# Performance work log

Measured on AMD Instinct MI355X. Metric: run time of the kernel, lower is better.

Reference implementation:

```python
import jax, jax.numpy as jnp
import numpy as np

N = 100000      # num_nodes
R = 8           # num_relations
D = 128         # node feature size
EMB = 128       # embedding_size
E = 1600000     # num edges
B = 16384       # batch of triples


def setup_inputs() -> dict:
    key = jax.random.key(0)
    ks = jax.random.split(key, 10)
    edge_src = jax.random.randint(ks[0], (E,), 0, N, dtype=jnp.int32)
    edge_dst = jax.random.randint(ks[1], (E,), 0, N, dtype=jnp.int32)
    edge_rel = jax.random.randint(ks[2], (E,), 0, R, dtype=jnp.int32)
    tri_nodes = jax.random.randint(ks[3], (B, 2), 0, N, dtype=jnp.int32)
    tri_rel = jax.random.randint(ks[4], (B,), 0, R, dtype=jnp.int32)
    X = jax.random.normal(ks[5], (N, D), dtype=jnp.float32)            # frozen node features
    W_rel = jax.random.normal(ks[6], (R, D, EMB), dtype=jnp.float32) * (1.0 / np.sqrt(D))
    W_self = jax.random.normal(ks[7], (D, EMB), dtype=jnp.float32) * (1.0 / np.sqrt(D))
    b = jnp.zeros((EMB,), dtype=jnp.float32)
    rel_emb = jax.random.normal(ks[8], (R, EMB), dtype=jnp.float32) * (1.0 / np.sqrt(EMB))  # xavier-ish
    return {"X": X, "W_rel": W_rel, "W_self": W_self, "b": b, "rel_emb": rel_emb,
            "edge_src": edge_src, "edge_dst": edge_dst, "edge_rel": edge_rel,
            "tri_nodes": tri_nodes, "tri_rel": tri_rel}


def _rgcn_layer(X, W_rel, W_self, b, edge_src, edge_dst, edge_rel):
    # per-relation transformed features: [R, N, EMB]
    XW = jnp.einsum('nd,rde->rne', X, W_rel)
    # gather per-edge messages: [E, EMB]
    msg = XW[edge_rel, edge_src]
    # RGCN normalization 1/c_{i,r}: count of (dst, rel) pairs
    comb = edge_dst.astype(jnp.int32) * R + edge_rel
    cnt = jax.ops.segment_sum(jnp.ones_like(comb, dtype=jnp.float32), comb, num_segments=N * R)
    norm = 1.0 / jnp.maximum(cnt[comb], 1.0)
    agg = jax.ops.segment_sum(msg * norm[:, None], edge_dst, num_segments=N)  # [N, EMB]
    return jax.nn.relu(agg + X @ W_self + b)


def reference(X, W_rel, W_self, b, rel_emb, edge_src, edge_dst, edge_rel, tri_nodes, tri_rel):
    H = _rgcn_layer(X, W_rel, W_self, b, edge_src, edge_dst, edge_rel)  # [N, EMB]
    subj = H[tri_nodes[:, 0]]          # [B, EMB]
    obj = H[tri_nodes[:, 1]]           # [B, EMB]
    rel = rel_emb[tri_rel]             # [B, EMB]
    scores = jnp.sum(subj * rel * obj, axis=1, keepdims=True)  # [B, 1]
    return scores
```

## Files before the change

kernel.cpp:

```cpp
#include <hip/hip_runtime.h>

typedef float f32x4 __attribute__((ext_vector_type(4)));
typedef short bf16x8 __attribute__((ext_vector_type(8)));

__device__ __forceinline__ unsigned short f2bf(float f) {
  unsigned int u = __float_as_uint(f);
  u += 0x7FFFu + ((u >> 16) & 1u);
  return (unsigned short)(u >> 16);
}
__device__ __forceinline__ float bflo(unsigned int u) {
  return __uint_as_float(u << 16);
}
__device__ __forceinline__ float bfhi(unsigned int u) {
  return __uint_as_float(u & 0xFFFF0000u);
}

__global__ void k_build_map(const int* __restrict__ tri_nodes, int* __restrict__ map,
                            int* __restrict__ uniq, int* __restrict__ counter, int n) {
  int i = blockIdx.x * blockDim.x + threadIdx.x;
  if (i >= n) return;
  int node = tri_nodes[i];
  int old = atomicCAS(&map[node], -1, -2);
  if (old == -1) {
    int mid = atomicAdd(counter, 1);
    uniq[mid] = node;
    map[node] = mid;
  }
}

__global__ void k_count(const int* __restrict__ edst, const int* __restrict__ erel,
                        const int* __restrict__ map, int* __restrict__ cnt_c, int E) {
  int i = blockIdx.x * blockDim.x + threadIdx.x;
  if (i >= E) return;
  int mid = map[edst[i]];
  if (mid >= 0) atomicAdd(&cnt_c[mid * 8 + erel[i]], 1);
}

__global__ __launch_bounds__(256) void k_scan_s1(const int* __restrict__ cnt_c,
                                                 int* __restrict__ bsum) {
  __shared__ int sh[256];
  int tid = threadIdx.x;
  int base = blockIdx.x * 1024 + tid * 4;
  int s = cnt_c[base] + cnt_c[base + 1] + cnt_c[base + 2] + cnt_c[base + 3];
  sh[tid] = s;
  __syncthreads();
  for (int o = 1; o < 256; o <<= 1) {
    int x = (tid >= o) ? sh[tid - o] : 0;
    __syncthreads();
    sh[tid] += x;
    __syncthreads();
  }
  if (tid == 255) bsum[blockIdx.x] = sh[255];
}
__global__ __launch_bounds__(256) void k_scan_s2(int* __restrict__ bsum,
                                                 int* __restrict__ seg_start, int M) {
  __shared__ int sh[256];
  int tid = threadIdx.x;
  int v = bsum[tid];
  sh[tid] = v;
  __syncthreads();
  for (int o = 1; o < 256; o <<= 1) {
    int x = (tid >= o) ? sh[tid - o] : 0;
    __syncthreads();
    sh[tid] += x;
    __syncthreads();
  }
  bsum[tid] = sh[tid] - v;
  if (tid == 255) seg_start[M] = sh[255];
}
__global__ __launch_bounds__(256) void k_scan_s3(const int* __restrict__ cnt_c,
                                                 const int* __restrict__ bsum,
                                                 int* __restrict__ seg_start,
                                                 int* __restrict__ seg_ofs) {
  __shared__ int sh[256];
  int tid = threadIdx.x;
  int base = blockIdx.x * 1024 + tid * 4;
  int c0 = cnt_c[base], c1 = cnt_c[base + 1], c2 = cnt_c[base + 2], c3 = cnt_c[base + 3];
  int s = c0 + c1 + c2 + c3;
  sh[tid] = s;
  __syncthreads();
  for (int o = 1; o < 256; o <<= 1) {
    int x = (tid >= o) ? sh[tid - o] : 0;
    __syncthreads();
    sh[tid] += x;
    __syncthreads();
  }
  int run = bsum[blockIdx.x] + sh[tid] - s;
  seg_start[base] = run; seg_ofs[base] = run; run += c0;
  seg_start[base + 1] = run; seg_ofs[base + 1] = run; run += c1;
  seg_start[base + 2] = run; seg_ofs[base + 2] = run; run += c2;
  seg_start[base + 3] = run; seg_ofs[base + 3] = run;
}

__global__ void k_scatter(const int* __restrict__ esrc, const int* __restrict__ edst,
                          const int* __restrict__ erel, const int* __restrict__ map,
                          int* __restrict__ seg_ofs, int* __restrict__ s_src, int E) {
  int i = blockIdx.x * blockDim.x + threadIdx.x;
  if (i >= E) return;
  int mid = map[edst[i]];
  if (mid >= 0) {
    int comb = mid * 8 + erel[i];
    int pos = atomicAdd(&seg_ofs[comb], 1);
    s_src[pos] = esrc[i];
  }
}

__global__ void k_cvt_w(const float* __restrict__ W_rel, const float* __restrict__ W_self,
                        unsigned short* __restrict__ Wf) {
  int i = blockIdx.x * 256 + threadIdx.x;
  if (i >= 9 * 16384) return;
  int j = i & 7;
  int tmp = i >> 3;
  int col = tmp & 127;
  int ku = (tmp >> 7) & 15;
  int r = tmp >> 11;
  int d = ku * 8 + j;
  float v = (r < 8) ? W_rel[r * 16384 + d * 128 + col] : W_self[d * 128 + col];
  Wf[i] = f2bf(v);
}

__global__ void k_cvt_x(const float* __restrict__ X, unsigned short* __restrict__ X16,
                        int total8) {
  int i = blockIdx.x * 256 + threadIdx.x;
  if (i >= total8) return;
  const float4* s = (const float4*)(X + (size_t)i * 8);
  float4 v0 = s[0], v1 = s[1];
  uint4 p;
  p.x = (unsigned int)f2bf(v0.x) | ((unsigned int)f2bf(v0.y) << 16);
  p.y = (unsigned int)f2bf(v0.z) | ((unsigned int)f2bf(v0.w) << 16);
  p.z = (unsigned int)f2bf(v1.x) | ((unsigned int)f2bf(v1.y) << 16);
  p.w = (unsigned int)f2bf(v1.z) | ((unsigned int)f2bf(v1.w) << 16);
  ((uint4*)X16)[i] = p;
}

template <int XMODE>
__global__ __launch_bounds__(256) void k_fused(
    const float* __restrict__ X, const unsigned short* __restrict__ X16,
    const unsigned short* __restrict__ Wf, const float* __restrict__ bvec,
    const int* __restrict__ uniq, const int* __restrict__ counter,
    const int* __restrict__ seg_start, const int* __restrict__ s_src,
    float* __restrict__ Hacc) {
  __shared__ __align__(16) unsigned short a_lds[16 * 128];
  __shared__ int lds_src[768];

  int nm = *counter;
  int mid0 = blockIdx.x * 16;
  if (mid0 >= nm) return;

  int t = threadIdx.x;
  int er = t >> 4, seg = t & 15;
  int lane = t & 63, l15 = lane & 15, lg = lane >> 4;
  int wc = t >> 6;
  int mid = mid0 + er;

  int i0 = seg_start[mid0 * 8];
  int range = seg_start[mid0 * 8 + 128] - i0;
  for (int j = t; j < range && j < 768; j += 256) lds_src[j] = s_src[i0 + j];
  bool fits = (range <= 768);

  f32x4 acc[2];
  {
    f32x4 z = {0.f, 0.f, 0.f, 0.f};
    acc[0] = z; acc[1] = z;
  }

  for (int r = 0; r < 9; ++r) {
    __syncthreads();

    {
      float aa[8];
#pragma unroll
      for (int q = 0; q < 8; ++q) aa[q] = 0.f;

      auto addrow = [&](int sidx) {
        if (XMODE == 0) {
          const float4* xr = (const float4*)(X + (size_t)sidx * 128) + seg * 2;
          float4 v0 = xr[0], v1 = xr[1];
          aa[0] += v0.x; aa[1] += v0.y; aa[2] += v0.z; aa[3] += v0.w;
          aa[4] += v1.x; aa[5] += v1.y; aa[6] += v1.z; aa[7] += v1.w;
        } else {
          uint4 u = *(const uint4*)(X16 + (size_t)sidx * 128 + seg * 8);
          aa[0] += bflo(u.x); aa[1] += bfhi(u.x);
          aa[2] += bflo(u.y); aa[3] += bfhi(u.y);
          aa[4] += bflo(u.z); aa[5] += bfhi(u.z);
          aa[6] += bflo(u.w); aa[7] += bfhi(u.w);
        }
      };

      if (r < 8) {
        int comb = mid * 8 + r;
        int s0 = seg_start[comb], s1 = seg_start[comb + 1];
        int cnt = s1 - s0;
        if (fits) {
          int o = s0 - i0, oe = s1 - i0;
          for (; o + 2 <= oe; o += 2) {
            int ia = lds_src[o], ib = lds_src[o + 1];
            addrow(ia);
            addrow(ib);
          }
          if (o < oe) addrow(lds_src[o]);
        } else {
          int e = s0;
          for (; e + 2 <= s1; e += 2) {
            int ia = s_src[e], ib = s_src[e + 1];
            addrow(ia);
            addrow(ib);
          }
          if (e < s1) addrow(s_src[e]);
        }
        if (cnt > 1) {
          float sc = 1.0f / (float)cnt;
#pragma unroll
          for (int q = 0; q < 8; ++q) aa[q] *= sc;
        }
      } else if (mid < nm) {
        addrow(uniq[mid]);
      }
      uint4 p;
      p.x = (unsigned int)f2bf(aa[0]) | ((unsigned int)f2bf(aa[1]) << 16);
      p.y = (unsigned int)f2bf(aa[2]) | ((unsigned int)f2bf(aa[3]) << 16);
      p.z = (unsigned int)f2bf(aa[4]) | ((unsigned int)f2bf(aa[5]) << 16);
      p.w = (unsigned int)f2bf(aa[6]) | ((unsigned int)f2bf(aa[7]) << 16);
      *(uint4*)&a_lds[(((er * 16 + seg) ^ (er & 7)) * 8)] = p;
    }
    __syncthreads();

    const unsigned short* wf = Wf + r * 16384;
#pragma unroll
    for (int kb = 0; kb < 4; ++kb) {
      int ku = kb * 4 + lg;
      bf16x8 af = *(const bf16x8*)&a_lds[((l15 * 16 + ku) ^ (l15 & 7)) * 8];
#pragma unroll
      for (int n = 0; n < 2; ++n) {
        int col = wc * 32 + n * 16 + l15;
        bf16x8 bfr = *(const bf16x8*)(wf + ((size_t)(ku * 128 + col)) * 8);
        acc[n] = __builtin_amdgcn_mfma_f32_16x16x32_bf16(af, bfr, acc[n], 0, 0, 0);
      }
    }
  }

#pragma unroll
  for (int n = 0; n < 2; ++n) {
    int col = wc * 32 + n * 16 + l15;
    float bv = bvec[col];
#pragma unroll
    for (int q = 0; q < 4; ++q) {
      int row = mid0 + lg * 4 + q;
      float v = acc[n][q] + bv;
      Hacc[(size_t)row * 128 + col] = v > 0.f ? v : 0.f;
    }
  }
}

__global__ void k_score(const float* __restrict__ H, const int* __restrict__ map,
                        const float* __restrict__ rel_emb, const int* __restrict__ tri_nodes,
                        const int* __restrict__ tri_rel, float* __restrict__ out, int B) {
  int w = (blockIdx.x * blockDim.x + threadIdx.x) >> 6;
  int lane = threadIdx.x & 63;
  if (w >= B) return;
  int s = map[tri_nodes[w * 2]];
  int o = map[tri_nodes[w * 2 + 1]];
  const float* hs = H + (size_t)s * 128;
  const float* ho = H + (size_t)o * 128;
  const float* rr = rel_emb + (size_t)tri_rel[w] * 128;
  float p = hs[lane] * ho[lane] * rr[lane] + hs[lane + 64] * ho[lane + 64] * rr[lane + 64];
#pragma unroll
  for (int ofs = 32; ofs > 0; ofs >>= 1) p += __shfl_down(p, ofs);
  if (lane == 0) out[w] = p;
}

extern "C" void kernel_launch(void* const* d_in, const int* in_sizes, int n_in,
                              void* d_out, int out_size, void* d_ws, size_t ws_size,
                              hipStream_t stream) {
  const float* X       = (const float*)d_in[0];
  const float* W_rel   = (const float*)d_in[1];
  const float* W_self  = (const float*)d_in[2];
  const float* bvec    = (const float*)d_in[3];
  const float* rel_emb = (const float*)d_in[4];
  const int* edge_src  = (const int*)d_in[5];
  const int* edge_dst  = (const int*)d_in[6];
  const int* edge_rel  = (const int*)d_in[7];
  const int* tri_nodes = (const int*)d_in[8];
  const int* tri_rel   = (const int*)d_in[9];

  int N  = in_sizes[0] / 128;
  int E  = in_sizes[5];
  int nt = in_sizes[8];
  int B  = in_sizes[9];
  int M  = nt * 8;

  char* ws = (char*)d_ws;
  int* map       = (int*)ws;
  int* counter   = map + N;
  int* uniq      = counter + 64;
  int* cnt_c     = uniq + nt;
  int* seg_start = cnt_c + M;
  int* seg_ofs   = seg_start + M + 64;
  int* bsum      = seg_ofs + M;
  int* s_src     = bsum + 256;
  float* Hacc    = (float*)(s_src + E);
  unsigned short* Wf  = (unsigned short*)cnt_c;
  unsigned short* X16 = (unsigned short*)(Hacc + (size_t)nt * 128);
  size_t need_big = ((char*)(X16 + (size_t)N * 128)) - ws;
  bool bigws = ws_size >= need_big;

  hipMemsetAsync(map, 0xFF, (size_t)N * 4, stream);
  hipMemsetAsync(counter, 0, 64 * 4, stream);
  hipMemsetAsync(cnt_c, 0, (size_t)M * 4, stream);

  int eblocks = (E + 255) / 256;
  k_build_map<<<(nt + 255) / 256, 256, 0, stream>>>(tri_nodes, map, uniq, counter, nt);
  k_count<<<eblocks, 256, 0, stream>>>(edge_dst, edge_rel, map, cnt_c, E);
  k_scan_s1<<<256, 256, 0, stream>>>(cnt_c, bsum);
  k_scan_s2<<<1, 256, 0, stream>>>(bsum, seg_start, M);
  k_scan_s3<<<256, 256, 0, stream>>>(cnt_c, bsum, seg_start, seg_ofs);
  k_cvt_w<<<(9 * 16384 + 255) / 256, 256, 0, stream>>>(W_rel, W_self, Wf);
  k_scatter<<<eblocks, 256, 0, stream>>>(edge_src, edge_dst, edge_rel, map, seg_ofs,
                                         s_src, E);
  if (bigws) {
    k_cvt_x<<<(N * 16 + 255) / 256, 256, 0, stream>>>(X, X16, N * 16);
    k_fused<1><<<nt / 16, 256, 0, stream>>>(X, X16, Wf, bvec, uniq, counter,
                                            seg_start, s_src, Hacc);
  } else {
    k_fused<0><<<nt / 16, 256, 0, stream>>>(X, X16, Wf, bvec, uniq, counter,
                                            seg_start, s_src, Hacc);
  }
  k_score<<<(B * 64 + 255) / 256, 256, 0, stream>>>(Hacc, map, rel_emb, tri_nodes,
                                                    tri_rel, (float*)d_out, B);
}
```

Before: 132.9 us.

## Fuse X bf16 conversion into count pass and compact edges for scatter

```diff
diff --git a/kernel.cpp b/kernel.cpp
--- a/kernel.cpp
+++ b/kernel.cpp
@@ -28,12 +28,42 @@
   }
 }
 
-__global__ void k_count(const int* __restrict__ edst, const int* __restrict__ erel,
-                        const int* __restrict__ map, int* __restrict__ cnt_c, int E) {
-  int i = blockIdx.x * blockDim.x + threadIdx.x;
-  if (i >= E) return;
-  int mid = map[edst[i]];
-  if (mid >= 0) atomicAdd(&cnt_c[mid * 8 + erel[i]], 1);
+__global__ void k_count(const int* __restrict__ esrc, const int* __restrict__ edst,
+                        const int* __restrict__ erel, const int* __restrict__ map,
+                        int* __restrict__ cnt_c, int E,
+                        const float* __restrict__ X, unsigned short* __restrict__ X16,
+                        int total8, int2* __restrict__ c_pk, int* __restrict__ wcount) {
+  int t = threadIdx.x;
+  int i = blockIdx.x * 256 + t;
+  if (i < total8) {
+    const float4* s = (const float4*)(X + (size_t)i * 8);
+    float4 v0 = s[0], v1 = s[1];
+    uint4 p;
+    p.x = (unsigned int)f2bf(v0.x) | ((unsigned int)f2bf(v0.y) << 16);
+    p.y = (unsigned int)f2bf(v0.z) | ((unsigned int)f2bf(v0.w) << 16);
+    p.z = (unsigned int)f2bf(v1.x) | ((unsigned int)f2bf(v1.y) << 16);
+    p.w = (unsigned int)f2bf(v1.z) | ((unsigned int)f2bf(v1.w) << 16);
+    ((uint4*)X16)[i] = p;
+  }
+  bool valid = false;
+  int comb = 0, src = 0;
+  if (i < E) {
+    int mid = map[edst[i]];
+    if (mid >= 0) {
+      valid = true;
+      comb = mid * 8 + erel[i];
+      src = esrc[i];
+      atomicAdd(&cnt_c[comb], 1);
+    }
+  }
+  unsigned long long m = __ballot(valid);
+  int lane = t & 63;
+  int w = (blockIdx.x << 2) + (t >> 6);
+  if (valid) {
+    int rank = (int)__popcll(m & ((1ull << lane) - 1ull));
+    c_pk[w * 64 + rank] = make_int2(comb, src);
+  }
+  if (lane == 0) wcount[w] = (int)__popcll(m);
 }
 
 __global__ __launch_bounds__(256) void k_scan_s1(const int* __restrict__ cnt_c,
@@ -92,6 +122,20 @@
   seg_start[base + 3] = run; seg_ofs[base + 3] = run;
 }
 
+__global__ void k_scatter2(const int2* __restrict__ c_pk, const int* __restrict__ wcount,
+                           int* __restrict__ seg_ofs, int* __restrict__ s_src,
+                           int nwaves) {
+  int t = threadIdx.x;
+  int w = blockIdx.x * 4 + (t >> 6);
+  if (w >= nwaves) return;
+  int lane = t & 63;
+  if (lane < wcount[w]) {
+    int2 p = c_pk[w * 64 + lane];
+    int pos = atomicAdd(&seg_ofs[p.x], 1);
+    s_src[pos] = p.y;
+  }
+}
+
 __global__ void k_scatter(const int* __restrict__ esrc, const int* __restrict__ edst,
                           const int* __restrict__ erel, const int* __restrict__ map,
                           int* __restrict__ seg_ofs, int* __restrict__ s_src, int E) {
@@ -117,20 +161,6 @@
   int d = ku * 8 + j;
   float v = (r < 8) ? W_rel[r * 16384 + d * 128 + col] : W_self[d * 128 + col];
   Wf[i] = f2bf(v);
-}
-
-__global__ void k_cvt_x(const float* __restrict__ X, unsigned short* __restrict__ X16,
-                        int total8) {
-  int i = blockIdx.x * 256 + threadIdx.x;
-  if (i >= total8) return;
-  const float4* s = (const float4*)(X + (size_t)i * 8);
-  float4 v0 = s[0], v1 = s[1];
-  uint4 p;
-  p.x = (unsigned int)f2bf(v0.x) | ((unsigned int)f2bf(v0.y) << 16);
-  p.y = (unsigned int)f2bf(v0.z) | ((unsigned int)f2bf(v0.w) << 16);
-  p.z = (unsigned int)f2bf(v1.x) | ((unsigned int)f2bf(v1.y) << 16);
-  p.w = (unsigned int)f2bf(v1.z) | ((unsigned int)f2bf(v1.w) << 16);
-  ((uint4*)X16)[i] = p;
 }
 
 template <int XMODE>
@@ -288,6 +318,8 @@
   int nt = in_sizes[8];
   int B  = in_sizes[9];
   int M  = nt * 8;
+  int eblocks = (E + 255) / 256;
+  int nwaves = eblocks * 4;
 
   char* ws = (char*)d_ws;
   int* map       = (int*)ws;
@@ -297,31 +329,40 @@
   int* seg_start = cnt_c + M;
   int* seg_ofs   = seg_start + M + 64;
   int* bsum      = seg_ofs + M;
-  int* s_src     = bsum + 256;
+  int* wcount    = bsum + 256;
+  int* s_src     = wcount + nwaves + 64;
   float* Hacc    = (float*)(s_src + E);
   unsigned short* Wf  = (unsigned short*)cnt_c;
   unsigned short* X16 = (unsigned short*)(Hacc + (size_t)nt * 128);
-  size_t need_big = ((char*)(X16 + (size_t)N * 128)) - ws;
+  int2* c_pk = (int2*)(X16 + (size_t)N * 128);
+  size_t need_big = ((char*)(c_pk + E)) - ws;
   bool bigws = ws_size >= need_big;
 
   hipMemsetAsync(map, 0xFF, (size_t)N * 4, stream);
   hipMemsetAsync(counter, 0, 64 * 4, stream);
   hipMemsetAsync(cnt_c, 0, (size_t)M * 4, stream);
 
-  int eblocks = (E + 255) / 256;
   k_build_map<<<(nt + 255) / 256, 256, 0, stream>>>(tri_nodes, map, uniq, counter, nt);
-  k_count<<<eblocks, 256, 0, stream>>>(edge_dst, edge_rel, map, cnt_c, E);
+  if (bigws) {
+    k_count<<<eblocks, 256, 0, stream>>>(edge_src, edge_dst, edge_rel, map, cnt_c, E,
+                                         X, X16, N * 16, c_pk, wcount);
+  } else {
+    k_count<<<eblocks, 256, 0, stream>>>(edge_src, edge_dst, edge_rel, map, cnt_c, E,
+                                         X, (unsigned short*)Hacc , 0,
+                                         (int2*)Hacc ,
+                                         wcount);
+  }
   k_scan_s1<<<256, 256, 0, stream>>>(cnt_c, bsum);
   k_scan_s2<<<1, 256, 0, stream>>>(bsum, seg_start, M);
   k_scan_s3<<<256, 256, 0, stream>>>(cnt_c, bsum, seg_start, seg_ofs);
   k_cvt_w<<<(9 * 16384 + 255) / 256, 256, 0, stream>>>(W_rel, W_self, Wf);
-  k_scatter<<<eblocks, 256, 0, stream>>>(edge_src, edge_dst, edge_rel, map, seg_ofs,
-                                         s_src, E);
   if (bigws) {
-    k_cvt_x<<<(N * 16 + 255) / 256, 256, 0, stream>>>(X, X16, N * 16);
+    k_scatter2<<<eblocks, 256, 0, stream>>>(c_pk, wcount, seg_ofs, s_src, nwaves);
     k_fused<1><<<nt / 16, 256, 0, stream>>>(X, X16, Wf, bvec, uniq, counter,
                                             seg_start, s_src, Hacc);
   } else {
+    k_scatter<<<eblocks, 256, 0, stream>>>(edge_src, edge_dst, edge_rel, map, seg_ofs,
+                                           s_src, E);
     k_fused<0><<<nt / 16, 256, 0, stream>>>(X, X16, Wf, bvec, uniq, counter,
                                             seg_start, s_src, Hacc);
   }
```

Result: faster. 128.2 us (-3.6%).
